# Optimization experiments

Measured on AMD Instinct MI355X. Metric: run time of the kernel, lower is better.

Reference implementation:

```python
import jax, jax.numpy as jnp
import numpy as np

NITERS = 5


def setup_inputs() -> dict:
    key = jax.random.key(0)
    k1, k2, k3 = jax.random.split(key, 3)
    bs, ncls, r, c = 4, 21, 64, 64
    n = r * c
    seg = jax.random.normal(k1, (bs, ncls, r, c), dtype=jnp.float32)
    W = jax.random.uniform(k2, (bs, n, n), dtype=jnp.float32)  # positive affinities
    weights = jax.random.normal(k3, (ncls, ncls), dtype=jnp.float32)  # learned compat matrix (init eye in torch)
    return {"seg": seg, "W": W, "weights": weights}


def reference(seg, W, weights):
    bs, d, r, c = seg.shape
    n = r * c
    qVals = seg.reshape(bs, d, n)
    uniqs = qVals
    # D[i] = diag(1 / W[i].sum(1)) @ W[i]  ==  row-normalized W (broadcast divide)
    D = W / W.sum(axis=2, keepdims=True)  # [bs, n, n]
    for _ in range(NITERS):
        Q = jax.nn.softmax(qVals, axis=1)                    # softmax over class dim
        seg_diff = jnp.einsum('bdn,bmn->bdm', Q, D)          # Q @ D^T -> [bs, d, n]
        seg_update = jnp.einsum('de,ben->bdn', weights, seg_diff)
        qVals = uniqs - seg_update
    return qVals.reshape(bs, d, r, c)
```

## Files before the change

kernel.cpp:

```cpp
#include <hip/hip_runtime.h>
#include <math.h>


#define DC 21
#define DCP 32
#define NN 4096
#define BS 4

typedef unsigned int u32;
typedef unsigned short u16;
typedef unsigned char u8;
typedef float f4v __attribute__((ext_vector_type(4)));

typedef __attribute__((address_space(1))) const unsigned int as1_u32;
typedef __attribute__((address_space(3))) unsigned int as3_u32;

#define WAITVM(n) asm volatile("s_waitcnt vmcnt(" #n ")" ::: "memory")

__device__ __forceinline__ u16 f2bf(float f) {
    u32 u = __float_as_uint(f);
    u = u + 0x7fffu + ((u >> 16) & 1u);
    return (u16)(u >> 16);
}

__device__ __forceinline__ u8 f2e4(float f) {
    if (!(f >= 0.015625f)) {
        int q = __float2int_rn(f * 512.0f);
        return (u8)q;
    }
    u32 b = __float_as_uint(f);
    b += 0x7FFFFu + ((b >> 20) & 1u);
    return (u8)(((((b >> 23) & 0xFFu) - 120u) << 3) | ((b >> 20) & 7u));
}

__global__ __launch_bounds__(64) void prep_k(const float* __restrict__ W,
                                             u8* __restrict__ D) {
    const int m = blockIdx.x;
    const int l = threadIdx.x;
    const float4* Wr = (const float4*)(W + (size_t)m * NN) + l;
    float4 v[16];
    float s = 0.f;
#pragma unroll
    for (int i = 0; i < 16; ++i) {
        v[i] = Wr[i * 64];
        s += (v[i].x + v[i].y) + (v[i].z + v[i].w);
    }
#pragma unroll
    for (int off = 1; off < 64; off <<= 1) s += __shfl_xor(s, off);
    const float inv2k = 2048.f / s;
    u32* Dr = (u32*)(D + (size_t)m * NN);
#pragma unroll
    for (int i = 0; i < 16; ++i) {
        u32 w = (u32)f2e4(v[i].x * inv2k) | ((u32)f2e4(v[i].y * inv2k) << 8) |
                ((u32)f2e4(v[i].z * inv2k) << 16) | ((u32)f2e4(v[i].w * inv2k) << 24);
        Dr[i * 64 + l] = w;
    }
}

__global__ __launch_bounds__(256) void softmax0_k(const float* __restrict__ x,
                                                  u8* __restrict__ q) {
    unsigned gid = blockIdx.x * 256u + threadIdx.x;
    unsigned b = gid >> 12, n = gid & 4095u;
    const float* xb = x + (size_t)b * DC * NN + n;
    float v[DC];
    float m = -1e30f;
#pragma unroll
    for (int d = 0; d < DC; ++d) { v[d] = xb[(size_t)d * NN]; m = fmaxf(m, v[d]); }
    float s = 0.f;
#pragma unroll
    for (int d = 0; d < DC; ++d) { v[d] = __expf(v[d] - m); s += v[d]; }
    float inv = 1.f / s;
    u8* qb = q + (size_t)b * DCP * NN + n;
#pragma unroll
    for (int d = 0; d < DC; ++d) qb[(size_t)d * NN] = f2e4(v[d] * inv);
}

__global__ __launch_bounds__(256, 2) void iter_k(const u8* __restrict__ Q,
                                                 const u8* __restrict__ D,
                                                 const float* __restrict__ wc,
                                                 const float* __restrict__ seg,
                                                 u8* __restrict__ qnext,
                                                 float* __restrict__ out,
                                                 int last) {
    __shared__ __align__(16) char lds[4][16384];
    __shared__ float wcs[DC * DC];
    float (*Cf)[2][16][DCP] = (float (*)[2][16][DCP])&lds[0][0];

    const int tid = threadIdx.x;
    const int w   = tid >> 6;
    const int l   = tid & 63;
    const int b   = blockIdx.x >> 7;
    const int m0  = (blockIdx.x & 127) * 32;

    for (int i = tid; i < DC * DC; i += 256)
        wcs[i] = wc[i] * (1.f / 2048.f);

    const int r  = l & 15;
    const int q4 = l >> 4;

    const u8* Db = D + ((size_t)b * NN + m0) * NN;
    const u8* Qb = Q + (size_t)b * DCP * NN;

    const int drow = l >> 4;
    const int dinn = (l & 15) * 16;

    f4v a00 = {0.f,0.f,0.f,0.f}, a01 = {0.f,0.f,0.f,0.f};
    f4v a10 = {0.f,0.f,0.f,0.f}, a11 = {0.f,0.f,0.f,0.f};

#define STAGE(c)                                                                     \
    {                                                                                \
        const int bi_ = (c) & 3;                                                     \
        _Pragma("unroll")                                                            \
        for (int ii = 0; ii < 2; ++ii) {                                             \
            const int i_   = w * 2 + ii;                                             \
            const int row_ = 4 * i_ + drow;                                          \
            const u8* ga = Db + (size_t)row_ * NN + (c) * 256                        \
                           + (dinn ^ ((row_ & 7) << 4));                             \
            __builtin_amdgcn_global_load_lds((as1_u32*)ga,                           \
                (as3_u32*)&lds[bi_][i_ * 1024], 16, 0, 0);                           \
            const u8* gb = Qb + (size_t)row_ * NN + (c) * 256                        \
                           + (dinn ^ ((row_ & 7) << 4));                             \
            __builtin_amdgcn_global_load_lds((as1_u32*)gb,                           \
                (as3_u32*)&lds[bi_][8192 + i_ * 1024], 16, 0, 0);                    \
        }                                                                            \
    }

    STAGE(0);
    STAGE(1);
    STAGE(2);

    const int swzr  = (r & 7) << 4;
    const int kbase = w * 64 + q4 * 8;

#pragma unroll
    for (int c = 0; c < 16; ++c) {
        if (c < 14) { WAITVM(8); }
        else if (c == 14) { WAITVM(4); }
        else { WAITVM(0); }
        __builtin_amdgcn_s_barrier();
        __builtin_amdgcn_sched_barrier(0);
        if (c + 3 < 16) STAGE(c + 3);

        const char* bufA = &lds[c & 3][0];
        const char* bufB = &lds[c & 3][8192];
#pragma unroll
        for (int ks = 0; ks < 2; ++ks) {
            const int off = kbase + ks * 32;
            long fa0 = *(const long*)&bufA[(r)      * 256 + (off ^ swzr)];
            long fa1 = *(const long*)&bufA[(16 + r) * 256 + (off ^ swzr)];
            long fbl = *(const long*)&bufB[(r)      * 256 + (off ^ swzr)];
            long fbh = *(const long*)&bufB[(16 + r) * 256 + (off ^ swzr)];
            a00 = __builtin_amdgcn_mfma_f32_16x16x32_fp8_fp8(fa0, fbl, a00, 0, 0, 0);
            a01 = __builtin_amdgcn_mfma_f32_16x16x32_fp8_fp8(fa0, fbh, a01, 0, 0, 0);
            a10 = __builtin_amdgcn_mfma_f32_16x16x32_fp8_fp8(fa1, fbl, a10, 0, 0, 0);
            a11 = __builtin_amdgcn_mfma_f32_16x16x32_fp8_fp8(fa1, fbh, a11, 0, 0, 0);
        }
    }
#undef STAGE

#pragma unroll
    for (int i = 0; i < 4; ++i) {
        Cf[w][0][q4 * 4 + i][r]      = a00[i];
        Cf[w][0][q4 * 4 + i][16 + r] = a01[i];
        Cf[w][1][q4 * 4 + i][r]      = a10[i];
        Cf[w][1][q4 * 4 + i][16 + r] = a11[i];
    }
    __syncthreads();

    const int row16 = tid >> 4;
    const int lg    = tid & 15;
#pragma unroll
    for (int pass = 0; pass < 2; ++pass) {
        const int m = m0 + pass * 16 + row16;

        float sd[24];
#pragma unroll
        for (int j = 0; j < 6; ++j) {
            float4 v = make_float4(0.f, 0.f, 0.f, 0.f);
#pragma unroll
            for (int w2 = 0; w2 < 4; ++w2) {
                float4 cc = *(const float4*)&Cf[w2][pass][row16][j * 4];
                v.x += cc.x; v.y += cc.y; v.z += cc.z; v.w += cc.w;
            }
            sd[j * 4 + 0] = v.x; sd[j * 4 + 1] = v.y;
            sd[j * 4 + 2] = v.z; sd[j * 4 + 3] = v.w;
        }

        const int d1 = lg;
        const int d2 = 16 + lg;
        float u1 = 0.f;
#pragma unroll
        for (int e = 0; e < DC; ++e) u1 += wcs[d1 * DC + e] * sd[e];
        float v1 = seg[((size_t)b * DC + d1) * NN + m] - u1;

        float v2 = -INFINITY;
        if (lg < 5) {
            float u2 = 0.f;
#pragma unroll
            for (int e = 0; e < DC; ++e) u2 += wcs[d2 * DC + e] * sd[e];
            v2 = seg[((size_t)b * DC + d2) * NN + m] - u2;
        }

        if (last) {
            out[((size_t)b * DC + d1) * NN + m] = v1;
            if (lg < 5) out[((size_t)b * DC + d2) * NN + m] = v2;
        } else {
            float mx = fmaxf(v1, v2);
#pragma unroll
            for (int off = 1; off < 16; off <<= 1) mx = fmaxf(mx, __shfl_xor(mx, off));
            float e1 = __expf(v1 - mx);
            float e2 = (lg < 5) ? __expf(v2 - mx) : 0.f;
            float ss = e1 + e2;
#pragma unroll
            for (int off = 1; off < 16; off <<= 1) ss += __shfl_xor(ss, off);
            float inv = 1.f / ss;
            qnext[((size_t)b * DCP + d1) * NN + m] = f2e4(e1 * inv);
            if (lg < 5) qnext[((size_t)b * DCP + d2) * NN + m] = f2e4(e2 * inv);
        }
    }
}

__global__ __launch_bounds__(256) void fb_softmax_k(const float* __restrict__ x,
                                                    float* __restrict__ q) {
    unsigned gid = blockIdx.x * 256u + threadIdx.x;
    unsigned b = gid >> 12, n = gid & 4095u;
    const float* xb = x + (size_t)b * DC * NN + n;
    float v[DC]; float m = -1e30f;
#pragma unroll
    for (int d = 0; d < DC; ++d) { v[d] = xb[(size_t)d * NN]; m = fmaxf(m, v[d]); }
    float s = 0.f;
#pragma unroll
    for (int d = 0; d < DC; ++d) { v[d] = __expf(v[d] - m); s += v[d]; }
    float inv = 1.f / s;
    float* qb = q + (size_t)b * DC * NN + n;
#pragma unroll
    for (int d = 0; d < DC; ++d) qb[(size_t)d * NN] = v[d] * inv;
}

__global__ __launch_bounds__(64) void fb_iter_k(const float* __restrict__ Q,
                                                const float* __restrict__ W,
                                                const float* __restrict__ wc,
                                                const float* __restrict__ seg,
                                                float* __restrict__ qnext,
                                                float* __restrict__ out,
                                                int write_q, int write_out) {
    const int lane = threadIdx.x;
    const int g = lane >> 4, l = lane & 15;
    const int b = blockIdx.x >> 9, rb = blockIdx.x & 511;
    const int m0 = rb * 8 + g * 2;
    const float4* Wr0 = (const float4*)(W + ((size_t)b * NN + m0) * NN + l * 4);
    const float4* Wr1 = (const float4*)(W + ((size_t)b * NN + m0 + 1) * NN + l * 4);
    const float4* Qf4 = (const float4*)(Q + (size_t)b * DC * NN + l * 4);
    float acc0[DC], acc1[DC];
#pragma unroll
    for (int d = 0; d < DC; ++d) { acc0[d] = 0.f; acc1[d] = 0.f; }
    float rs0 = 0.f, rs1 = 0.f;
#pragma unroll 2
    for (int s = 0; s < 64; ++s) {
        float4 wa = Wr0[s * 16], wb = Wr1[s * 16];
        rs0 += (wa.x + wa.y) + (wa.z + wa.w);
        rs1 += (wb.x + wb.y) + (wb.z + wb.w);
#pragma unroll
        for (int d = 0; d < DC; ++d) {
            float4 qv = Qf4[d * 1024 + s * 16];
            acc0[d] += qv.x * wa.x + qv.y * wa.y + qv.z * wa.z + qv.w * wa.w;
            acc1[d] += qv.x * wb.x + qv.y * wb.y + qv.z * wb.z + qv.w * wb.w;
        }
    }
#pragma unroll
    for (int off = 1; off < 16; off <<= 1) {
        rs0 += __shfl_xor(rs0, off); rs1 += __shfl_xor(rs1, off);
#pragma unroll
        for (int d = 0; d < DC; ++d) {
            acc0[d] += __shfl_xor(acc0[d], off);
            acc1[d] += __shfl_xor(acc1[d], off);
        }
    }
    const float inv0 = 1.f / rs0, inv1 = 1.f / rs1;
    const int d1 = l, d2 = l + 16;
    const bool has2 = (d2 < DC);
    float u0a = 0.f, u1a = 0.f, u0b = 0.f, u1b = 0.f;
#pragma unroll
    for (int e = 0; e < DC; ++e) {
        float w1 = wc[d1 * DC + e];
        u0a += w1 * acc0[e]; u1a += w1 * acc1[e];
    }
    if (has2) {
#pragma unroll
        for (int e = 0; e < DC; ++e) {
            float w2 = wc[d2 * DC + e];
            u0b += w2 * acc0[e]; u1b += w2 * acc1[e];
        }
    }
    const size_t base = (size_t)b * DC * NN;
    const size_t i0a = base + (size_t)d1 * NN + m0;
    const size_t i0b = base + (size_t)d2 * NN + m0;
    float v0a = seg[i0a] - u0a * inv0;
    float v1a = seg[i0a + 1] - u1a * inv1;
    float v0b = 0.f, v1b = 0.f;
    if (has2) { v0b = seg[i0b] - u0b * inv0; v1b = seg[i0b + 1] - u1b * inv1; }
    if (write_out) {
        out[i0a] = v0a; out[i0a + 1] = v1a;
        if (has2) { out[i0b] = v0b; out[i0b + 1] = v1b; }
    }
    if (write_q) {
        float mx0 = has2 ? fmaxf(v0a, v0b) : v0a;
        float mx1 = has2 ? fmaxf(v1a, v1b) : v1a;
#pragma unroll
        for (int off = 1; off < 16; off <<= 1) {
            mx0 = fmaxf(mx0, __shfl_xor(mx0, off));
            mx1 = fmaxf(mx1, __shfl_xor(mx1, off));
        }
        float e0a = __expf(v0a - mx0), e1a = __expf(v1a - mx1);
        float e0b = has2 ? __expf(v0b - mx0) : 0.f;
        float e1b = has2 ? __expf(v1b - mx1) : 0.f;
        float s0 = e0a + e0b, s1 = e1a + e1b;
#pragma unroll
        for (int off = 1; off < 16; off <<= 1) {
            s0 += __shfl_xor(s0, off); s1 += __shfl_xor(s1, off);
        }
        float is0 = 1.f / s0, is1 = 1.f / s1;
        qnext[i0a] = e0a * is0; qnext[i0a + 1] = e1a * is1;
        if (has2) { qnext[i0b] = e0b * is0; qnext[i0b + 1] = e1b * is1; }
    }
}

extern "C" void kernel_launch(void* const* d_in, const int* in_sizes, int n_in,
                              void* d_out, int out_size, void* d_ws, size_t ws_size,
                              hipStream_t stream) {
    const float* seg = (const float*)d_in[0];
    const float* W   = (const float*)d_in[1];
    const float* wc  = (const float*)d_in[2];
    float* out = (float*)d_out;

    const size_t needD = (size_t)BS * NN * NN * sizeof(u8);
    const size_t needQ = (size_t)BS * DCP * NN * sizeof(u8);

    if (ws_size >= needD + needQ && (size_t)out_size * sizeof(float) >= needQ) {
        u8* Dq = (u8*)d_ws;
        u8* Q0 = (u8*)((char*)d_ws + needD);
        u8* Q1 = (u8*)d_out;

        prep_k<<<dim3(BS * NN), dim3(64), 0, stream>>>(W, Dq);
        softmax0_k<<<dim3(BS * NN / 256), dim3(256), 0, stream>>>(seg, Q0);

        const u8* qin = Q0;
        u8* qout = Q1;
        for (int it = 0; it < 5; ++it) {
            iter_k<<<dim3(BS * NN / 32), dim3(256), 0, stream>>>(
                qin, Dq, wc, seg, qout, out, (it == 4) ? 1 : 0);
            const u8* t = qin; qin = qout; qout = (u8*)t;
        }
    } else {
        float* Qa = (float*)d_ws;
        float* Qb = Qa + (size_t)BS * DC * NN;
        fb_softmax_k<<<dim3(BS * NN / 256), dim3(256), 0, stream>>>(seg, Qa);
        const float* qin = Qa;
        float* qout = Qb;
        for (int it = 0; it < 5; ++it) {
            fb_iter_k<<<dim3(2048), dim3(64), 0, stream>>>(
                qin, W, wc, seg, qout, out, (it < 4) ? 1 : 0, (it == 4) ? 1 : 0);
            const float* t = qin; qin = qout; qout = (float*)t;
        }
    }
}
```

Measured before the change: 457.0 us.

## Fuse prep, softmax and all iterations into one cooperative persistent kernel

Adds a cooperative kernel in which each of 512 blocks loads its 32 rows of W once, converts them to fp8 and keeps them in registers for all five iterations. Row sums are folded in as a scale applied after the MFMA rather than baked into the stored matrix. Iterations are separated by grid-wide syncs, so the separate prep pass that wrote a 64MB fp8 D and the per-iteration re-reads of D are gone. It also switches to the hardware packed fp8 conversion builtin. The costs are a very high register footprint (64 longs per lane) that limits occupancy, grid sync overhead, and reliance on all 512 blocks being co-resident; if the cooperative launch fails, the old path runs instead.

```diff
diff --git a/kernel.cpp b/kernel.cpp
--- a/kernel.cpp
+++ b/kernel.cpp
@@ -1,5 +1,8 @@
 #include <hip/hip_runtime.h>
+#include <hip/hip_cooperative_groups.h>
 #include <math.h>
+
+namespace cg = cooperative_groups;
 
 
 #define DC 21
@@ -17,12 +20,6 @@
 
 #define WAITVM(n) asm volatile("s_waitcnt vmcnt(" #n ")" ::: "memory")
 
-__device__ __forceinline__ u16 f2bf(float f) {
-    u32 u = __float_as_uint(f);
-    u = u + 0x7fffu + ((u >> 16) & 1u);
-    return (u16)(u >> 16);
-}
-
 __device__ __forceinline__ u8 f2e4(float f) {
     if (!(f >= 0.015625f)) {
         int q = __float2int_rn(f * 512.0f);
@@ -31,6 +28,219 @@
     u32 b = __float_as_uint(f);
     b += 0x7FFFFu + ((b >> 20) & 1u);
     return (u8)(((((b >> 23) & 0xFFu) - 120u) << 3) | ((b >> 20) & 7u));
+}
+
+__device__ __forceinline__ u32 cvtpk4(float a, float b, float c, float d) {
+#if __has_builtin(__builtin_amdgcn_cvt_pk_fp8_f32)
+    u32 v = __builtin_amdgcn_cvt_pk_fp8_f32(a, b, 0u, false);
+    v = __builtin_amdgcn_cvt_pk_fp8_f32(c, d, v, true);
+    return v;
+#else
+    return (u32)f2e4(a) | ((u32)f2e4(b) << 8) |
+           ((u32)f2e4(c) << 16) | ((u32)f2e4(d) << 24);
+#endif
+}
+
+__device__ __forceinline__ u8 cvt1(float a) {
+#if __has_builtin(__builtin_amdgcn_cvt_pk_fp8_f32)
+    return (u8)(__builtin_amdgcn_cvt_pk_fp8_f32(a, 0.f, 0u, false) & 0xFFu);
+#else
+    return f2e4(a);
+#endif
+}
+
+__device__ __forceinline__ void qnextw(u8* q, int b, int d, int m, u8 v) {
+    q[((size_t)b * DCP + d) * NN + m] = v;
+}
+
+__global__ __launch_bounds__(256, 2) void fused_k(const float* __restrict__ seg,
+                                                  const float* __restrict__ W,
+                                                  const float* __restrict__ wc,
+                                                  u8* __restrict__ q0,
+                                                  u8* __restrict__ q1,
+                                                  float* __restrict__ out) {
+    __shared__ __align__(16) char bstage[4][2][8192];
+    __shared__ float wcs[DC * DC];
+    __shared__ float inv_rs[32];
+    __shared__ float rs_part[4][32];
+    float (*Cf)[2][16][DCP] = (float (*)[2][16][DCP])&bstage[0][0][0];
+
+    cg::grid_group grid = cg::this_grid();
+
+    const int tid = threadIdx.x;
+    const int w   = tid >> 6;
+    const int l   = tid & 63;
+    const int b   = blockIdx.x >> 7;
+    const int m0  = (blockIdx.x & 127) * 32;
+
+    const int r    = l & 15;
+    const int q4   = l >> 4;
+    const int drow = l >> 4;
+    const int dinn = (l & 15) * 16;
+
+    for (int i = tid; i < DC * DC; i += 256) wcs[i] = wc[i];
+
+    if (tid < 32) {
+        const int col = blockIdx.x * 32 + tid;
+        const int bb = col >> 12, n = col & 4095;
+        const float* xb = seg + (size_t)bb * DC * NN + n;
+        float v[DC];
+        float mx = -1e30f;
+#pragma unroll
+        for (int d = 0; d < DC; ++d) { v[d] = xb[(size_t)d * NN]; mx = fmaxf(mx, v[d]); }
+        float s = 0.f;
+#pragma unroll
+        for (int d = 0; d < DC; ++d) { v[d] = __expf(v[d] - mx); s += v[d]; }
+        const float inv = 1.f / s;
+        u8* qb = q0 + (size_t)bb * DCP * NN + n;
+#pragma unroll
+        for (int d = 0; d < DC; ++d) qb[(size_t)d * NN] = cvt1(v[d] * inv);
+    }
+
+    long dreg[64];
+    const float* Wb = W + ((size_t)(b * NN + m0)) * NN + w * 1024 + q4 * 8;
+    float s0 = 0.f, s1 = 0.f;
+#pragma unroll
+    for (int row2 = 0; row2 < 2; ++row2) {
+        const float* Wr = Wb + (size_t)(row2 * 16 + r) * NN;
+#pragma unroll
+        for (int ks = 0; ks < 32; ++ks) {
+            float4 va = *(const float4*)(Wr + ks * 32);
+            float4 vb = *(const float4*)(Wr + ks * 32 + 4);
+            float sm = ((va.x + va.y) + (va.z + va.w)) +
+                       ((vb.x + vb.y) + (vb.z + vb.w));
+            if (row2 == 0) s0 += sm; else s1 += sm;
+            u32 lo = cvtpk4(va.x, va.y, va.z, va.w);
+            u32 hi = cvtpk4(vb.x, vb.y, vb.z, vb.w);
+            dreg[row2 * 32 + ks] = (long)(((unsigned long)hi << 32) | (unsigned long)lo);
+        }
+    }
+    s0 += __shfl_xor(s0, 16); s0 += __shfl_xor(s0, 32);
+    s1 += __shfl_xor(s1, 16); s1 += __shfl_xor(s1, 32);
+    if (l < 16) { rs_part[w][r] = s0; rs_part[w][16 + r] = s1; }
+    __syncthreads();
+    if (tid < 32) {
+        const float rsum = rs_part[0][tid] + rs_part[1][tid] +
+                           rs_part[2][tid] + rs_part[3][tid];
+        inv_rs[tid] = 1.f / rsum;
+    }
+
+    __threadfence();
+    grid.sync();
+
+    const u8* qin = q0;
+    u8* qout = q1;
+    const int swzr = (r & 7) << 4;
+
+    for (int it = 0; it < 5; ++it) {
+        const int lastit = (it == 4);
+        const u8* Qb = qin + (size_t)b * DCP * NN + w * 1024;
+
+#define QSTAGE(c)                                                                   \
+        {                                                                           \
+            _Pragma("unroll")                                                       \
+            for (int i_ = 0; i_ < 8; ++i_) {                                        \
+                const int cls_ = 4 * i_ + drow;                                     \
+                const u8* gq = Qb + (size_t)cls_ * NN + (c) * 256                   \
+                               + (dinn ^ ((cls_ & 7) << 4));                        \
+                __builtin_amdgcn_global_load_lds((as1_u32*)gq,                      \
+                    (as3_u32*)&bstage[w][(c) & 1][i_ * 1024], 16, 0, 0);            \
+            }                                                                       \
+        }
+
+        f4v a00 = {0.f,0.f,0.f,0.f}, a01 = {0.f,0.f,0.f,0.f};
+        f4v a10 = {0.f,0.f,0.f,0.f}, a11 = {0.f,0.f,0.f,0.f};
+
+        QSTAGE(0);
+#pragma unroll
+        for (int c = 0; c < 4; ++c) {
+            if (c < 3) { QSTAGE(c + 1); WAITVM(8); }
+            else       { WAITVM(0); }
+            __builtin_amdgcn_sched_barrier(0);
+            const char* bufB = &bstage[w][c & 1][0];
+#pragma unroll
+            for (int ks = 0; ks < 8; ++ks) {
+                const int off = ks * 32 + q4 * 8;
+                long fbl = *(const long*)&bufB[r        * 256 + (off ^ swzr)];
+                long fbh = *(const long*)&bufB[(16 + r) * 256 + (off ^ swzr)];
+                const int ki = c * 8 + ks;
+                a00 = __builtin_amdgcn_mfma_f32_16x16x32_fp8_fp8(dreg[ki],      fbl, a00, 0, 0, 0);
+                a01 = __builtin_amdgcn_mfma_f32_16x16x32_fp8_fp8(dreg[ki],      fbh, a01, 0, 0, 0);
+                a10 = __builtin_amdgcn_mfma_f32_16x16x32_fp8_fp8(dreg[32 + ki], fbl, a10, 0, 0, 0);
+                a11 = __builtin_amdgcn_mfma_f32_16x16x32_fp8_fp8(dreg[32 + ki], fbh, a11, 0, 0, 0);
+            }
+        }
+#undef QSTAGE
+
+        __syncthreads();
+#pragma unroll
+        for (int i = 0; i < 4; ++i) {
+            Cf[w][0][q4 * 4 + i][r]      = a00[i];
+            Cf[w][0][q4 * 4 + i][16 + r] = a01[i];
+            Cf[w][1][q4 * 4 + i][r]      = a10[i];
+            Cf[w][1][q4 * 4 + i][16 + r] = a11[i];
+        }
+        __syncthreads();
+
+        const int row16 = tid >> 4;
+        const int lg    = tid & 15;
+#pragma unroll
+        for (int pass = 0; pass < 2; ++pass) {
+            const int m = m0 + pass * 16 + row16;
+            const float ir = inv_rs[pass * 16 + row16];
+
+            float sd[24];
+#pragma unroll
+            for (int j = 0; j < 6; ++j) {
+                float4 v = make_float4(0.f, 0.f, 0.f, 0.f);
+#pragma unroll
+                for (int w2 = 0; w2 < 4; ++w2) {
+                    float4 cc = *(const float4*)&Cf[w2][pass][row16][j * 4];
+                    v.x += cc.x; v.y += cc.y; v.z += cc.z; v.w += cc.w;
+                }
+                sd[j * 4 + 0] = v.x; sd[j * 4 + 1] = v.y;
+                sd[j * 4 + 2] = v.z; sd[j * 4 + 3] = v.w;
+            }
+
+            const int d1 = lg;
+            const int d2 = 16 + lg;
+            float u1 = 0.f;
+#pragma unroll
+            for (int e = 0; e < DC; ++e) u1 += wcs[d1 * DC + e] * sd[e];
+            float v1 = seg[((size_t)b * DC + d1) * NN + m] - u1 * ir;
+
+            float v2 = -INFINITY;
+            if (lg < 5) {
+                float u2 = 0.f;
+#pragma unroll
+                for (int e = 0; e < DC; ++e) u2 += wcs[d2 * DC + e] * sd[e];
+                v2 = seg[((size_t)b * DC + d2) * NN + m] - u2 * ir;
+            }
+
+            if (lastit) {
+                out[((size_t)b * DC + d1) * NN + m] = v1;
+                if (lg < 5) out[((size_t)b * DC + d2) * NN + m] = v2;
+            } else {
+                float mx = fmaxf(v1, v2);
+#pragma unroll
+                for (int off = 1; off < 16; off <<= 1) mx = fmaxf(mx, __shfl_xor(mx, off));
+                float e1 = __expf(v1 - mx);
+                float e2 = (lg < 5) ? __expf(v2 - mx) : 0.f;
+                float ss = e1 + e2;
+#pragma unroll
+                for (int off = 1; off < 16; off <<= 1) ss += __shfl_xor(ss, off);
+                float inv = 1.f / ss;
+                qnextw(qout, b, d1, m, cvt1(e1 * inv));
+                if (lg < 5) qnextw(qout, b, d2, m, cvt1(e2 * inv));
+            }
+        }
+
+        if (!lastit) {
+            __threadfence();
+            grid.sync();
+            const u8* t = qin; qin = qout; qout = (u8*)t;
+        }
+    }
 }
 
 __global__ __launch_bounds__(64) void prep_k(const float* __restrict__ W,
@@ -51,9 +261,8 @@
     u32* Dr = (u32*)(D + (size_t)m * NN);
 #pragma unroll
     for (int i = 0; i < 16; ++i) {
-        u32 w = (u32)f2e4(v[i].x * inv2k) | ((u32)f2e4(v[i].y * inv2k) << 8) |
-                ((u32)f2e4(v[i].z * inv2k) << 16) | ((u32)f2e4(v[i].w * inv2k) << 24);
-        Dr[i * 64 + l] = w;
+        Dr[i * 64 + l] = cvtpk4(v[i].x * inv2k, v[i].y * inv2k,
+                                v[i].z * inv2k, v[i].w * inv2k);
     }
 }
 
@@ -72,7 +281,7 @@
     float inv = 1.f / s;
     u8* qb = q + (size_t)b * DCP * NN + n;
 #pragma unroll
-    for (int d = 0; d < DC; ++d) qb[(size_t)d * NN] = f2e4(v[d] * inv);
+    for (int d = 0; d < DC; ++d) qb[(size_t)d * NN] = cvt1(v[d] * inv);
 }
 
 __global__ __launch_bounds__(256, 2) void iter_k(const u8* __restrict__ Q,
@@ -214,8 +423,8 @@
 #pragma unroll
             for (int off = 1; off < 16; off <<= 1) ss += __shfl_xor(ss, off);
             float inv = 1.f / ss;
-            qnext[((size_t)b * DCP + d1) * NN + m] = f2e4(e1 * inv);
-            if (lg < 5) qnext[((size_t)b * DCP + d2) * NN + m] = f2e4(e2 * inv);
+            qnext[((size_t)b * DCP + d1) * NN + m] = cvt1(e1 * inv);
+            if (lg < 5) qnext[((size_t)b * DCP + d2) * NN + m] = cvt1(e2 * inv);
         }
     }
 }
@@ -336,7 +545,21 @@
     const size_t needD = (size_t)BS * NN * NN * sizeof(u8);
     const size_t needQ = (size_t)BS * DCP * NN * sizeof(u8);
 
-    if (ws_size >= needD + needQ && (size_t)out_size * sizeof(float) >= needQ) {
+    bool done = false;
+
+    if (ws_size >= needQ && (size_t)out_size * sizeof(float) >= needQ) {
+        u8* q0 = (u8*)d_ws;
+        u8* q1 = (u8*)d_out;
+        void* args[6] = {(void*)&seg, (void*)&W, (void*)&wc,
+                         (void*)&q0, (void*)&q1, (void*)&out};
+        hipError_t e = hipLaunchCooperativeKernel((const void*)fused_k,
+                                                  dim3(512), dim3(256),
+                                                  args, 0, stream);
+        done = (e == hipSuccess);
+    }
+
+    if (!done && ws_size >= needD + needQ &&
+        (size_t)out_size * sizeof(float) >= needQ) {
         u8* Dq = (u8*)d_ws;
         u8* Q0 = (u8*)((char*)d_ws + needD);
         u8* Q1 = (u8*)d_out;
@@ -351,7 +574,10 @@
                 qin, Dq, wc, seg, qout, out, (it == 4) ? 1 : 0);
             const u8* t = qin; qin = qout; qout = (u8*)t;
         }
-    } else {
+        done = true;
+    }
+
+    if (!done) {
         float* Qa = (float*)d_ws;
         float* Qb = Qa + (size_t)BS * DC * NN;
         fb_softmax_k<<<dim3(BS * NN / 256), dim3(256), 0, stream>>>(seg, Qa);
```

New measurement: 1.029 ms. 125% more time.
